# Kernel optimization log

Measured on AMD Instinct MI355X. Metric: run time of the kernel, lower is better.

Reference implementation:

```python
import functools
import jax, jax.numpy as jnp
import numpy as np

INPUT_DIM = 3
NUM_LEVELS = 8
LEVEL_DIM = 2
PER_LEVEL_SCALE = 2
BASE_RESOLUTION = 16
LOG2_HASHMAP_SIZE = 19
BATCH = 2_097_152

PRIMES = np.array([1, 2654435761, 805459861], dtype=np.uint32)


def _level_offsets():
    max_params = 2 ** LOG2_HASHMAP_SIZE
    offsets, offset = [], 0
    for i in range(NUM_LEVELS):
        res = int(np.ceil(BASE_RESOLUTION * PER_LEVEL_SCALE ** i))
        params = min(max_params, res ** INPUT_DIM)
        params = int(np.ceil(params / 32) * 32)
        offset += params
        offsets.append(offset)
    return offsets  # cumulative, last entry = total table rows


OFFSETS = _level_offsets()
TABLE_ROWS = OFFSETS[-1]  # 2920448


def setup_inputs() -> dict:
    key = jax.random.key(0)
    k1, k2 = jax.random.split(key)
    inputs = jax.random.uniform(k1, (BATCH, INPUT_DIM), dtype=jnp.float32)
    embeddings = jax.random.normal(k2, (TABLE_ROWS, LEVEL_DIM), dtype=jnp.float32) * 0.05
    return {"inputs": inputs, "embeddings": embeddings}


def reference(inputs, embeddings):
    primes = jnp.asarray(PRIMES)  # uint32; multiply wraps mod 2^32, matching `& 0xFFFFFFFF`
    outs = []
    for i in range(NUM_LEVELS):
        res = int(np.ceil(BASE_RESOLUTION * PER_LEVEL_SCALE ** i))
        offset = 0 if i == 0 else OFFSETS[i - 1]
        params_in_level = OFFSETS[i] - offset
        x = inputs * res  # [N, 3], nonnegative
        xi = jnp.floor(x)  # == trunc for x >= 0, matches .long()
        xf = x - jax.lax.stop_gradient(xi)  # fractional part, grad flows only through x
        bin_mask = xf < 0.5  # eval-mode stochastic-corner: pick nearest corner
        xi_u = xi.astype(jnp.uint32)
        neigs = jnp.where(bin_mask, xi_u, xi_u + jnp.uint32(1))  # [N, 3]
        h = neigs * primes  # uint32 wraparound multiply
        hashed = functools.reduce(jnp.bitwise_xor, [h[..., d] for d in range(INPUT_DIM)])
        hash_ids = (hashed % jnp.uint32(params_in_level)).astype(jnp.int32) + offset  # [N]
        feats = embeddings[hash_ids]  # [N, level_dim] irregular gather
        w = jnp.where(bin_mask, xf, 1.0 - xf)  # [N, 3]
        outs.append(jnp.concatenate([feats, w], axis=-1))  # [N, level_dim + 3]
    outs.append(inputs)
    return jnp.concatenate(outs, axis=-1)  # [N, num_levels*(level_dim+3)+3] = [N, 43]
```

## Files before the change

### kernel.cpp

```cpp
#include <hip/hip_runtime.h>

#define NLEV 8
#define COLS 43
#define TPB 64

typedef float v4f __attribute__((ext_vector_type(4)));

__global__ __launch_bounds__(TPB) void hashgrid_kernel(
    const float* __restrict__ inputs,
    const float2* __restrict__ emb,
    float* __restrict__ out,
    int N)
{
    __shared__ __align__(16) float lds[TPB * COLS];
    const int tid = threadIdx.x;
    const int i = blockIdx.x * TPB + tid;

    const unsigned off_c[NLEV]  = {0u, 4096u, 36864u, 299008u,
                                   823296u, 1347584u, 1871872u, 2396160u};
    const unsigned mask_c[NLEV] = {4095u, 32767u, 262143u, 524287u,
                                   524287u, 524287u, 524287u, 524287u};

    if (i < N) {
        const float x0 = inputs[3 * i + 0];
        const float x1 = inputs[3 * i + 1];
        const float x2 = inputs[3 * i + 2];

        unsigned id[NLEV];
        float ga[NLEV], gb[NLEV], gc[NLEV];
        bool  ma[NLEV], mb[NLEV], mc[NLEV];
        #pragma unroll
        for (int L = 0; L < NLEV; ++L) {
            const float res = (float)(16 << L);
            const float a = x0 * res, b = x1 * res, c = x2 * res;
            const float fa = floorf(a), fb = floorf(b), fc = floorf(c);
            ga[L] = a - fa; gb[L] = b - fb; gc[L] = c - fc;
            ma[L] = ga[L] < 0.5f; mb[L] = gb[L] < 0.5f; mc[L] = gc[L] < 0.5f;
            const unsigned na = (unsigned)fa + (ma[L] ? 0u : 1u);
            const unsigned nb = (unsigned)fb + (mb[L] ? 0u : 1u);
            const unsigned nc = (unsigned)fc + (mc[L] ? 0u : 1u);
            const unsigned h = na ^ (nb * 2654435761u) ^ (nc * 805459861u);
            id[L] = (h & mask_c[L]) + off_c[L];
        }
        float2 f[NLEV];
        #pragma unroll
        for (int L = 0; L < NLEV; ++L) {
            f[L] = emb[id[L]];
        }

        float* row = &lds[tid * COLS];
        #pragma unroll
        for (int L = 0; L < NLEV; ++L) {
            row[5 * L + 2] = ma[L] ? ga[L] : 1.0f - ga[L];
            row[5 * L + 3] = mb[L] ? gb[L] : 1.0f - gb[L];
            row[5 * L + 4] = mc[L] ? gc[L] : 1.0f - gc[L];
        }
        row[40] = x0;
        row[41] = x1;
        row[42] = x2;

        #pragma unroll
        for (int L = 0; L < NLEV; ++L) {
            row[5 * L + 0] = f[L].x;
            row[5 * L + 1] = f[L].y;
        }
    }
    __syncthreads();

    const long long tile_base = (long long)blockIdx.x * (TPB * COLS);
    if ((blockIdx.x + 1) * TPB <= N) {
        v4f* __restrict__ out4 = (v4f*)(out + tile_base);
        const v4f* l4 = (const v4f*)lds;
        const int NV = TPB * COLS / 4;
        #pragma unroll
        for (int j = 0; j < 10; ++j) {
            const int k = tid + j * TPB;
            __builtin_nontemporal_store(l4[k], &out4[k]);
        }
        const int k = tid + 10 * TPB;
        if (k < NV) {
            __builtin_nontemporal_store(l4[k], &out4[k]);
        }
    } else {
        const int valid = N - blockIdx.x * TPB;
        const int NT = valid * COLS;
        for (int k = tid; k < NT; k += TPB) {
            out[tile_base + k] = lds[k];
        }
    }
}

extern "C" void kernel_launch(void* const* d_in, const int* in_sizes, int n_in,
                              void* d_out, int out_size, void* d_ws, size_t ws_size,
                              hipStream_t stream) {
    const float*  inputs = (const float*)d_in[0];
    const float2* emb    = (const float2*)d_in[1];
    float* out = (float*)d_out;
    const int N = in_sizes[0] / 3;
    const int grid = (N + TPB - 1) / TPB;
    hashgrid_kernel<<<grid, TPB, 0, stream>>>(inputs, emb, out, N);
}
```

Baseline: 539.6 us.

## Split hash-grid into per-level gather kernel and assemble kernel via workspace

Splits the fused kernel in two. The first kernel interleaves blocks by level, so consecutive blocks gather from the same level's table region, which should improve L2 locality for the scattered embedding reads. Results go to a level-major workspace, and a second kernel reads them back, recomputes the weights and writes the interleaved 43-column rows through LDS. In exchange it adds a workspace round trip (write then read of 8*N float2), re-reads the inputs eight times and adds a second launch. The fused kernel remains as a fallback when no workspace is available.

```diff
diff --git a/kernel.cpp b/kernel.cpp
--- a/kernel.cpp
+++ b/kernel.cpp
@@ -2,9 +2,107 @@
 
 #define NLEV 8
 #define COLS 43
-#define TPB 64
+#define TPB1 256
+#define TPB  64
 
 typedef float v4f __attribute__((ext_vector_type(4)));
+typedef float v2f __attribute__((ext_vector_type(2)));
+
+__device__ __constant__ unsigned off_c[NLEV]  = {0u, 4096u, 36864u, 299008u,
+                                                 823296u, 1347584u, 1871872u, 2396160u};
+__device__ __constant__ unsigned mask_c[NLEV] = {4095u, 32767u, 262143u, 524287u,
+                                                 524287u, 524287u, 524287u, 524287u};
+
+__global__ __launch_bounds__(TPB1) void gather_kernel(
+    const float* __restrict__ inputs,
+    const float2* __restrict__ emb,
+    v2f* __restrict__ ws,
+    int N)
+{
+    const int level = blockIdx.x & 7;
+    const int i = (blockIdx.x >> 3) * TPB1 + threadIdx.x;
+    if (i >= N) return;
+
+    const float x0 = __builtin_nontemporal_load(&inputs[3 * i + 0]);
+    const float x1 = __builtin_nontemporal_load(&inputs[3 * i + 1]);
+    const float x2 = __builtin_nontemporal_load(&inputs[3 * i + 2]);
+
+    const float res = (float)(16 << level);
+    const float a = x0 * res, b = x1 * res, c = x2 * res;
+    const float fa = floorf(a), fb = floorf(b), fc = floorf(c);
+    const float ga = a - fa, gb = b - fb, gc = c - fc;
+    const unsigned na = (unsigned)fa + (ga < 0.5f ? 0u : 1u);
+    const unsigned nb = (unsigned)fb + (gb < 0.5f ? 0u : 1u);
+    const unsigned nc = (unsigned)fc + (gc < 0.5f ? 0u : 1u);
+    const unsigned h = na ^ (nb * 2654435761u) ^ (nc * 805459861u);
+    const unsigned id = (h & mask_c[level]) + off_c[level];
+
+    const float2 f = emb[id];
+    v2f v; v.x = f.x; v.y = f.y;
+    __builtin_nontemporal_store(v, ws + (size_t)level * N + i);
+}
+
+__global__ __launch_bounds__(TPB) void assemble_kernel(
+    const float* __restrict__ inputs,
+    const v2f* __restrict__ ws,
+    float* __restrict__ out,
+    int N)
+{
+    __shared__ __align__(16) float lds[TPB * COLS];
+    const int tid = threadIdx.x;
+    const int i = blockIdx.x * TPB + tid;
+
+    if (i < N) {
+        v2f f[NLEV];
+        #pragma unroll
+        for (int L = 0; L < NLEV; ++L)
+            f[L] = __builtin_nontemporal_load(ws + (size_t)L * N + i);
+
+        const float x0 = inputs[3 * i + 0];
+        const float x1 = inputs[3 * i + 1];
+        const float x2 = inputs[3 * i + 2];
+        float* row = &lds[tid * COLS];
+
+        #pragma unroll
+        for (int L = 0; L < NLEV; ++L) {
+            const float res = (float)(16 << L);
+            const float a = x0 * res, b = x1 * res, c = x2 * res;
+            const float ga = a - floorf(a), gb = b - floorf(b), gc = c - floorf(c);
+            row[5 * L + 2] = ga < 0.5f ? ga : 1.0f - ga;
+            row[5 * L + 3] = gb < 0.5f ? gb : 1.0f - gb;
+            row[5 * L + 4] = gc < 0.5f ? gc : 1.0f - gc;
+        }
+        #pragma unroll
+        for (int L = 0; L < NLEV; ++L) {
+            row[5 * L + 0] = f[L].x;
+            row[5 * L + 1] = f[L].y;
+        }
+        row[40] = x0;
+        row[41] = x1;
+        row[42] = x2;
+    }
+    __syncthreads();
+
+    const long long tile_base = (long long)blockIdx.x * (TPB * COLS);
+    if ((blockIdx.x + 1) * TPB <= N) {
+        v4f* __restrict__ out4 = (v4f*)(out + tile_base);
+        const v4f* l4 = (const v4f*)lds;
+        const int NV = TPB * COLS / 4;
+        #pragma unroll
+        for (int j = 0; j < 10; ++j) {
+            const int k = tid + j * TPB;
+            __builtin_nontemporal_store(l4[k], &out4[k]);
+        }
+        const int k = tid + 10 * TPB;
+        if (k < NV)
+            __builtin_nontemporal_store(l4[k], &out4[k]);
+    } else {
+        const int valid = N - blockIdx.x * TPB;
+        const int NT = valid * COLS;
+        for (int k = tid; k < NT; k += TPB)
+            out[tile_base + k] = lds[k];
+    }
+}
 
 __global__ __launch_bounds__(TPB) void hashgrid_kernel(
     const float* __restrict__ inputs,
@@ -15,11 +113,6 @@
     __shared__ __align__(16) float lds[TPB * COLS];
     const int tid = threadIdx.x;
     const int i = blockIdx.x * TPB + tid;
-
-    const unsigned off_c[NLEV]  = {0u, 4096u, 36864u, 299008u,
-                                   823296u, 1347584u, 1871872u, 2396160u};
-    const unsigned mask_c[NLEV] = {4095u, 32767u, 262143u, 524287u,
-                                   524287u, 524287u, 524287u, 524287u};
 
     if (i < N) {
         const float x0 = inputs[3 * i + 0];
@@ -44,9 +137,7 @@
         }
         float2 f[NLEV];
         #pragma unroll
-        for (int L = 0; L < NLEV; ++L) {
-            f[L] = emb[id[L]];
-        }
+        for (int L = 0; L < NLEV; ++L) f[L] = emb[id[L]];
 
         float* row = &lds[tid * COLS];
         #pragma unroll
@@ -58,7 +149,6 @@
         row[40] = x0;
         row[41] = x1;
         row[42] = x2;
-
         #pragma unroll
         for (int L = 0; L < NLEV; ++L) {
             row[5 * L + 0] = f[L].x;
@@ -78,15 +168,13 @@
             __builtin_nontemporal_store(l4[k], &out4[k]);
         }
         const int k = tid + 10 * TPB;
-        if (k < NV) {
+        if (k < NV)
             __builtin_nontemporal_store(l4[k], &out4[k]);
-        }
     } else {
         const int valid = N - blockIdx.x * TPB;
         const int NT = valid * COLS;
-        for (int k = tid; k < NT; k += TPB) {
+        for (int k = tid; k < NT; k += TPB)
             out[tile_base + k] = lds[k];
-        }
     }
 }
 
@@ -97,6 +185,15 @@
     const float2* emb    = (const float2*)d_in[1];
     float* out = (float*)d_out;
     const int N = in_sizes[0] / 3;
-    const int grid = (N + TPB - 1) / TPB;
-    hashgrid_kernel<<<grid, TPB, 0, stream>>>(inputs, emb, out, N);
+
+    const size_t ws_need = (size_t)NLEV * N * sizeof(float2);
+    if (d_ws != nullptr && ws_size >= ws_need) {
+        const int chunks = (N + TPB1 - 1) / TPB1;
+        gather_kernel<<<chunks * NLEV, TPB1, 0, stream>>>(inputs, emb, (v2f*)d_ws, N);
+        const int grid2 = (N + TPB - 1) / TPB;
+        assemble_kernel<<<grid2, TPB, 0, stream>>>(inputs, (const v2f*)d_ws, out, N);
+    } else {
+        const int grid = (N + TPB - 1) / TPB;
+        hashgrid_kernel<<<grid, TPB, 0, stream>>>(inputs, emb, out, N);
+    }
 }
```

Measured after the change: 554.8 us. +2.8%, slower.

## Store features in column-major LDS and recompute weights during output write

Applied to the files above, without the earlier changes.

Shared memory now holds only gathered features and the raw inputs in a padded column-major layout (19 rows of stride 260) instead of the full 43-column row tile. The corner weights are recomputed from the inputs in the store loop, and the block size goes from 64 to 256 threads. This cuts LDS footprint per point and avoids bank-conflicting strided row writes. In exchange, every output element needs integer division and branching, so the store loop does far more ALU work and its LDS reads may diverge.

```diff
diff --git a/kernel.cpp b/kernel.cpp
--- a/kernel.cpp
+++ b/kernel.cpp
@@ -2,7 +2,8 @@
 
 #define NLEV 8
 #define COLS 43
-#define TPB 64
+#define TPB  256
+#define SMS  260
 
 typedef float v4f __attribute__((ext_vector_type(4)));
 
@@ -12,7 +13,7 @@
     float* __restrict__ out,
     int N)
 {
-    __shared__ __align__(16) float lds[TPB * COLS];
+    __shared__ float sm[19 * SMS];
     const int tid = threadIdx.x;
     const int i = blockIdx.x * TPB + tid;
 
@@ -27,18 +28,15 @@
         const float x2 = inputs[3 * i + 2];
 
         unsigned id[NLEV];
-        float ga[NLEV], gb[NLEV], gc[NLEV];
-        bool  ma[NLEV], mb[NLEV], mc[NLEV];
         #pragma unroll
         for (int L = 0; L < NLEV; ++L) {
             const float res = (float)(16 << L);
             const float a = x0 * res, b = x1 * res, c = x2 * res;
             const float fa = floorf(a), fb = floorf(b), fc = floorf(c);
-            ga[L] = a - fa; gb[L] = b - fb; gc[L] = c - fc;
-            ma[L] = ga[L] < 0.5f; mb[L] = gb[L] < 0.5f; mc[L] = gc[L] < 0.5f;
-            const unsigned na = (unsigned)fa + (ma[L] ? 0u : 1u);
-            const unsigned nb = (unsigned)fb + (mb[L] ? 0u : 1u);
-            const unsigned nc = (unsigned)fc + (mc[L] ? 0u : 1u);
+            const float ga = a - fa, gb = b - fb, gc = c - fc;
+            const unsigned na = (unsigned)fa + (ga < 0.5f ? 0u : 1u);
+            const unsigned nb = (unsigned)fb + (gb < 0.5f ? 0u : 1u);
+            const unsigned nc = (unsigned)fc + (gc < 0.5f ? 0u : 1u);
             const unsigned h = na ^ (nb * 2654435761u) ^ (nc * 805459861u);
             id[L] = (h & mask_c[L]) + off_c[L];
         }
@@ -48,45 +46,65 @@
             f[L] = emb[id[L]];
         }
 
-        float* row = &lds[tid * COLS];
+        sm[16 * SMS + tid] = x0;
+        sm[17 * SMS + tid] = x1;
+        sm[18 * SMS + tid] = x2;
         #pragma unroll
         for (int L = 0; L < NLEV; ++L) {
-            row[5 * L + 2] = ma[L] ? ga[L] : 1.0f - ga[L];
-            row[5 * L + 3] = mb[L] ? gb[L] : 1.0f - gb[L];
-            row[5 * L + 4] = mc[L] ? gc[L] : 1.0f - gc[L];
-        }
-        row[40] = x0;
-        row[41] = x1;
-        row[42] = x2;
-
-        #pragma unroll
-        for (int L = 0; L < NLEV; ++L) {
-            row[5 * L + 0] = f[L].x;
-            row[5 * L + 1] = f[L].y;
+            sm[(2 * L + 0) * SMS + tid] = f[L].x;
+            sm[(2 * L + 1) * SMS + tid] = f[L].y;
         }
     }
     __syncthreads();
 
+    auto elem = [&](int k) -> float {
+        const unsigned uk = (unsigned)k;
+        const unsigned r = uk / 43u;
+        const unsigned c = uk - 43u * r;
+        if (c >= 40u) {
+            return sm[(16u + (c - 40u)) * SMS + r];
+        }
+        const unsigned L = c / 5u;
+        const unsigned s = c - 5u * L;
+        if (s < 2u) {
+            return sm[(2u * L + s) * SMS + r];
+        }
+        const unsigned axis = s - 2u;
+        const float x = sm[(16u + axis) * SMS + r];
+        const float res = (float)(16u << L);
+        const float a = x * res;
+        const float g = a - floorf(a);
+        return g < 0.5f ? g : 1.0f - g;
+    };
+
     const long long tile_base = (long long)blockIdx.x * (TPB * COLS);
     if ((blockIdx.x + 1) * TPB <= N) {
         v4f* __restrict__ out4 = (v4f*)(out + tile_base);
-        const v4f* l4 = (const v4f*)lds;
         const int NV = TPB * COLS / 4;
         #pragma unroll
         for (int j = 0; j < 10; ++j) {
-            const int k = tid + j * TPB;
-            __builtin_nontemporal_store(l4[k], &out4[k]);
+            const int k4 = tid + j * TPB;
+            v4f v;
+            v.x = elem(4 * k4 + 0);
+            v.y = elem(4 * k4 + 1);
+            v.z = elem(4 * k4 + 2);
+            v.w = elem(4 * k4 + 3);
+            __builtin_nontemporal_store(v, &out4[k4]);
         }
-        const int k = tid + 10 * TPB;
-        if (k < NV) {
-            __builtin_nontemporal_store(l4[k], &out4[k]);
+        const int k4 = tid + 10 * TPB;
+        if (k4 < NV) {
+            v4f v;
+            v.x = elem(4 * k4 + 0);
+            v.y = elem(4 * k4 + 1);
+            v.z = elem(4 * k4 + 2);
+            v.w = elem(4 * k4 + 3);
+            __builtin_nontemporal_store(v, &out4[k4]);
         }
     } else {
         const int valid = N - blockIdx.x * TPB;
         const int NT = valid * COLS;
-        for (int k = tid; k < NT; k += TPB) {
-            out[tile_base + k] = lds[k];
-        }
+        for (int k = tid; k < NT; k += TPB)
+            out[tile_base + k] = elem(k);
     }
 }
 
```

After: 542.1 us. Within noise of the previous version (+0.5%).
